# Performance work log

Measured on AMD Instinct MI355X. Metric: run time of the kernel, lower is better.

The kernel has to match this reference:

```python
import jax, jax.numpy as jnp
import numpy as np

D_MODEL = 1024
NUM_EXPERTS = 16
TOP_K = 2
TOP_C = 4  # min(M, max(4, 2*K))
RANK = 64  # max(4, d_model // 16) per choose_lowrank_r
TAU = 1.0


def setup_inputs() -> dict:
    key = jax.random.key(0)
    ks = jax.random.split(key, 7)
    B = 32768
    x = jax.random.normal(ks[0], (B, D_MODEL), dtype=jnp.float32)
    # shared encoder Linear(d, d) with bias
    We = jax.random.normal(ks[1], (D_MODEL, D_MODEL), dtype=jnp.float32) / np.sqrt(D_MODEL)
    be = jnp.zeros((D_MODEL,), dtype=jnp.float32)
    # gating Linear(d, M), no bias
    Wg = jax.random.normal(ks[2], (NUM_EXPERTS, D_MODEL), dtype=jnp.float32) / np.sqrt(D_MODEL)
    # per-expert LoRA weights: U: [M, r, d], V: [M, d, r], gamma: [M]
    U = jax.random.normal(ks[3], (NUM_EXPERTS, RANK, D_MODEL), dtype=jnp.float32) / np.sqrt(D_MODEL)
    V = jax.random.normal(ks[4], (NUM_EXPERTS, D_MODEL, RANK), dtype=jnp.float32) / np.sqrt(RANK)
    gamma = jnp.ones((NUM_EXPERTS,), dtype=jnp.float32)
    return {"x": x, "We": We, "be": be, "Wg": Wg, "U": U, "V": V, "gamma": gamma}


def reference(x, We, be, Wg, U, V, gamma):
    B = x.shape[0]
    encoded = x @ We.T + be                       # [B, d]
    logits = (encoded @ Wg.T) / TAU               # [B, M]
    # Top-C candidate selection, then Top-K among candidates
    topc_vals, topc_idx = jax.lax.top_k(logits, TOP_C)          # [B, C]
    topk_vals, pos_in_c = jax.lax.top_k(topc_vals, TOP_K)       # [B, K]
    topk_idx = jnp.take_along_axis(topc_idx, pos_in_c, axis=1)  # [B, K]
    # masked stable softmax over selected logits (matches _stable_masked_softmax)
    e = jnp.exp(topk_vals - jnp.max(topk_vals, axis=1, keepdims=True))
    w = e / (jnp.sum(e, axis=1, keepdims=True) + 1e-12)
    w = jnp.where(w > 1e-12, w, 0.0)  # keep_mask: drop negligible weights
    # scatter routing weights into dense [B, M] combine matrix
    w_full = jnp.zeros((B, NUM_EXPERTS), x.dtype).at[
        jnp.arange(B)[:, None], topk_idx].add(w)
    # expert residual delta: E(x) = x + gamma * V @ silu(U @ x)
    hidden = jax.nn.silu(jnp.einsum('bd,mrd->bmr', encoded, U))  # [B, M, r]
    delta = jnp.einsum('bmr,mdr,bm->bd', hidden, V, w_full * gamma[None, :])
    # y = encoded + sum_k w_k * (E_k(encoded) - encoded); sum_k w_k = 1
    return encoded + delta
```

## Files before the change

kernel.cpp:

```cpp
#include <hip/hip_runtime.h>
#include <stdint.h>

#define B_TOK 32768
#define DM 1024
#define NEXP 16
#define RK 64
#define NPAIR 256
#define TPT 64
#define HT 128
#define GRID_CMB 3072
#define GRID_HID 544
#define MAXTILE 1024

typedef unsigned short u16;
typedef __bf16 bf16x8 __attribute__((ext_vector_type(8)));
typedef float f32x4 __attribute__((ext_vector_type(4)));

__device__ __forceinline__ u16 f2bf(float f) {
  union { float f; uint32_t u; } v; v.f = f;
  return (u16)((v.u + 0x7fffu + ((v.u >> 16) & 1u)) >> 16);
}
__device__ __forceinline__ float bf2f(u16 u) {
  union { uint32_t i; float f; } v; v.i = ((uint32_t)u) << 16; return v.f;
}

__device__ __forceinline__ void gload_lds16(const void* g, void* l) {
  __builtin_amdgcn_global_load_lds(
      (const __attribute__((address_space(1))) void*)g,
      (__attribute__((address_space(3))) void*)l, 16, 0, 0);
}

__global__ void k_convert3(const float* __restrict__ s0, u16* __restrict__ d0,
                           const float* __restrict__ s1, u16* __restrict__ d1,
                           const float* __restrict__ s2, u16* __restrict__ d2) {
  const int seg = blockIdx.x >> 8;
  const int bid = blockIdx.x & 255;
  const float* src = (seg == 0) ? s0 : (seg == 1) ? s1 : s2;
  u16* dst = (seg == 0) ? d0 : (seg == 1) ? d1 : d2;
  int i = bid * 256 + threadIdx.x;
  #pragma unroll
  for (int v = 0; v < 4; ++v) {
    int idx = i + v * 65536;
    float4 f = reinterpret_cast<const float4*>(src)[idx];
    ushort4 o;
    o.x = f2bf(f.x); o.y = f2bf(f.y); o.z = f2bf(f.z); o.w = f2bf(f.w);
    reinterpret_cast<ushort4*>(dst)[idx] = o;
  }
}

__global__ void k_wgeff(const float* __restrict__ Wg, const float* __restrict__ We,
                        const float* __restrict__ be,
                        float* __restrict__ Wgeff, float* __restrict__ gbias) {
  int e = blockIdx.y;
  int d = blockIdx.x * 256 + threadIdx.x;
  double acc = 0.0;
  for (int k = 0; k < DM; ++k)
    acc += (double)Wg[e * DM + k] * (double)We[k * DM + d];
  Wgeff[e * DM + d] = (float)acc;
  if (blockIdx.x == 0 && threadIdx.x == 0) {
    double s = 0.0;
    for (int k = 0; k < DM; ++k) s += (double)be[k] * (double)Wg[e * DM + k];
    gbias[e] = (float)s;
  }
}

#define GT 64
#define GD 128

__global__ __launch_bounds__(256) void k_gating(
    const float* __restrict__ x, u16* __restrict__ x_bf,
    const float* __restrict__ Wgeff, const float* __restrict__ gbias,
    const float* __restrict__ gamma,
    int* __restrict__ tk_pid, float* __restrict__ tk_w0, float* __restrict__ tk_w1,
    int* __restrict__ counts_p, int* __restrict__ counts_e) {
  __shared__ float xs[GT][GD + 4];
  __shared__ float wsd[NEXP][GD + 4];
  __shared__ float lg[GT][NEXP + 2];
  __shared__ int bcnt[NPAIR];
  __shared__ int bexp[NEXP];
  const int tid = threadIdx.x;
  const int tok0 = blockIdx.x * GT;
  const int t0 = (tid >> 3) * 2;
  const int e0 = (tid & 7) * 2;
  bcnt[tid] = 0;
  if (tid < NEXP) bexp[tid] = 0;

  double acc00 = 0.0, acc01 = 0.0, acc10 = 0.0, acc11 = 0.0;

  for (int c = 0; c < DM; c += GD) {
    __syncthreads();
    #pragma unroll
    for (int v = 0; v < (GT * GD / 4) / 256; ++v) {
      int idx = tid + v * 256;
      int r = idx >> 5, cc = idx & 31;
      float4 v4 = *reinterpret_cast<const float4*>(x + (size_t)(tok0 + r) * DM + c + cc * 4);
      *reinterpret_cast<float4*>(&xs[r][cc * 4]) = v4;
      ushort4 o;
      o.x = f2bf(v4.x); o.y = f2bf(v4.y); o.z = f2bf(v4.z); o.w = f2bf(v4.w);
      *reinterpret_cast<ushort4*>(x_bf + (size_t)(tok0 + r) * DM + c + cc * 4) = o;
    }
    #pragma unroll
    for (int v = 0; v < (NEXP * GD / 4) / 256; ++v) {
      int idx = tid + v * 256;
      int r = idx >> 5, cc = idx & 31;
      *reinterpret_cast<float4*>(&wsd[r][cc * 4]) =
          *reinterpret_cast<const float4*>(Wgeff + (size_t)r * DM + c + cc * 4);
    }
    __syncthreads();
    #pragma unroll 8
    for (int d = 0; d < GD; d += 4) {
      float4 xa = *reinterpret_cast<const float4*>(&xs[t0][d]);
      float4 xb = *reinterpret_cast<const float4*>(&xs[t0 + 1][d]);
      float4 wa = *reinterpret_cast<const float4*>(&wsd[e0][d]);
      float4 wb = *reinterpret_cast<const float4*>(&wsd[e0 + 1][d]);
      acc00 += (double)xa.x * wa.x + (double)xa.y * wa.y + (double)xa.z * wa.z + (double)xa.w * wa.w;
      acc01 += (double)xa.x * wb.x + (double)xa.y * wb.y + (double)xa.z * wb.z + (double)xa.w * wb.w;
      acc10 += (double)xb.x * wa.x + (double)xb.y * wa.y + (double)xb.z * wa.z + (double)xb.w * wa.w;
      acc11 += (double)xb.x * wb.x + (double)xb.y * wb.y + (double)xb.z * wb.z + (double)xb.w * wb.w;
    }
  }

  lg[t0][e0]         = (float)(acc00 + (double)gbias[e0]);
  lg[t0][e0 + 1]     = (float)(acc01 + (double)gbias[e0 + 1]);
  lg[t0 + 1][e0]     = (float)(acc10 + (double)gbias[e0]);
  lg[t0 + 1][e0 + 1] = (float)(acc11 + (double)gbias[e0 + 1]);
  __syncthreads();

  if (tid < GT) {
    int tok = tok0 + tid;
    float v0 = lg[tid][0]; int i0 = 0;
    #pragma unroll
    for (int j = 1; j < NEXP; ++j)
      if (lg[tid][j] > v0) { v0 = lg[tid][j]; i0 = j; }
    float v1 = -3.4e38f; int i1 = 0;
    #pragma unroll
    for (int j = 0; j < NEXP; ++j) {
      if (j == i0) continue;
      if (lg[tid][j] > v1) { v1 = lg[tid][j]; i1 = j; }
    }
    float e1 = expf(v1 - v0);
    float denom = 1.0f + e1 + 1e-12f;
    float w0 = 1.0f / denom, w1 = e1 / denom;
    if (!(w0 > 1e-12f)) w0 = 0.0f;
    if (!(w1 > 1e-12f)) w1 = 0.0f;
    int pid = i0 * 16 + i1;
    tk_pid[tok] = pid;
    tk_w0[tok] = w0 * gamma[i0];
    tk_w1[tok] = w1 * gamma[i1];
    atomicAdd(&bcnt[pid], 1);
    atomicAdd(&bexp[i0], 1);
    atomicAdd(&bexp[i1], 1);
  }
  __syncthreads();
  if (bcnt[tid] > 0) atomicAdd(&counts_p[tid], bcnt[tid]);
  if (tid < NEXP && bexp[tid] > 0) atomicAdd(&counts_e[tid], bexp[tid]);
}

__global__ __launch_bounds__(NPAIR) void k_scan(
    const int* __restrict__ counts_p, const int* __restrict__ counts_e,
    int* __restrict__ offs_p, int* __restrict__ curs_p,
    int* __restrict__ offs_e, int* __restrict__ curs_e,
    int* __restrict__ tp_pair, int* __restrict__ tp_loc, int* __restrict__ n_tp,
    int* __restrict__ th_exp, int* __restrict__ th_loc, int* __restrict__ n_th) {
  __shared__ int sc[NPAIR], st[NPAIR];
  __shared__ int seb[NEXP + 1], thb[NEXP + 1];
  const int tid = threadIdx.x;
  const int c = counts_p[tid];
  const int nt = (c + TPT - 1) / TPT;
  sc[tid] = c; st[tid] = nt;
  __syncthreads();
  for (int s = 1; s < NPAIR; s <<= 1) {
    int vc = 0, vt = 0;
    if (tid >= s) { vc = sc[tid - s]; vt = st[tid - s]; }
    __syncthreads();
    sc[tid] += vc; st[tid] += vt;
    __syncthreads();
  }
  const int offc = sc[tid] - c;
  const int offt = st[tid] - nt;
  offs_p[tid] = offc;
  curs_p[tid] = offc;
  if (tid == NPAIR - 1) { offs_p[NPAIR] = sc[tid]; n_tp[0] = st[tid]; }
  for (int q = 0; q < nt; ++q) { tp_pair[offt + q] = tid; tp_loc[offt + q] = q * TPT; }

  if (tid == 0) {
    int s = 0, s2 = 0;
    for (int e = 0; e < NEXP; ++e) {
      seb[e] = s; thb[e] = s2;
      int ce = counts_e[e];
      s += ce; s2 += (ce + HT - 1) / HT;
    }
    seb[NEXP] = s; thb[NEXP] = s2;
    n_th[0] = s2;
  }
  __syncthreads();
  if (tid <= NEXP) offs_e[tid] = seb[tid];
  if (tid < NEXP) {
    curs_e[tid] = seb[tid];
    int ce = counts_e[tid];
    int ntt = (ce + HT - 1) / HT;
    for (int q = 0; q < ntt; ++q) { th_exp[thb[tid] + q] = tid; th_loc[thb[tid] + q] = q * HT; }
  }
}

__global__ __launch_bounds__(256) void k_scatter(
    const int* __restrict__ tk_pid, const float* __restrict__ tk_w0,
    const float* __restrict__ tk_w1,
    int* __restrict__ curs_p, int* __restrict__ curs_e,
    int* __restrict__ a_tok, int* __restrict__ a_h0,
    int* __restrict__ a_h1,
    int* __restrict__ e_tok, float* __restrict__ e_w) {
  __shared__ int hp[NPAIR];
  __shared__ int he[NEXP];
  __shared__ int bp[NPAIR];
  __shared__ int beB[NEXP];
  const int tid = threadIdx.x;
  const int tok = blockIdx.x * 256 + tid;
  hp[tid] = 0;
  if (tid < NEXP) he[tid] = 0;
  __syncthreads();

  const int pid = tk_pid[tok];
  const int i0 = pid >> 4, i1 = pid & 15;
  const int rp = atomicAdd(&hp[pid], 1);
  const int r0 = atomicAdd(&he[i0], 1);
  const int r1 = atomicAdd(&he[i1], 1);
  __syncthreads();

  if (hp[tid] > 0) bp[tid] = atomicAdd(&curs_p[tid], hp[tid]);
  if (tid < NEXP && he[tid] > 0) beB[tid] = atomicAdd(&curs_e[tid], he[tid]);
  __syncthreads();

  const int posp = bp[pid] + rp;
  const int pos0 = beB[i0] + r0;
  const int pos1 = beB[i1] + r1;
  a_tok[posp] = tok;
  a_h0[posp] = pos0;
  a_h1[posp] = pos1;
  e_tok[pos0] = tok; e_w[pos0] = tk_w0[tok];
  e_tok[pos1] = tok; e_w[pos1] = tk_w1[tok];
}

__global__ __launch_bounds__(256) void k_encoder(
    const u16* __restrict__ A, const u16* __restrict__ Bm,
    const float* __restrict__ bias, u16* __restrict__ Cb) {
  __shared__ __align__(16) u16 As0[128 * 64];
  __shared__ __align__(16) u16 Bs0[128 * 64];
  __shared__ __align__(16) u16 As1[128 * 64];
  __shared__ __align__(16) u16 Bs1[128 * 64];
  const int nwg = gridDim.x * gridDim.y;
  const int orig = blockIdx.y * gridDim.x + blockIdx.x;
  const int qq = nwg >> 3;
  const int swz = (orig & 7) * qq + (orig >> 3);
  const int m0 = (swz / gridDim.x) * 128, n0 = (swz % gridDim.x) * 128;
  const int tid = threadIdx.x;
  const int lane = tid & 63, wave = tid >> 6;
  const int wr = wave >> 1, wc = wave & 1;
  const int lrow = lane & 15, lhi = lane >> 4;

  f32x4 acc[4][4];
  #pragma unroll
  for (int i = 0; i < 4; ++i)
    #pragma unroll
    for (int j = 0; j < 4; ++j) acc[i][j] = (f32x4){0.f, 0.f, 0.f, 0.f};

  const u16* gA0; const u16* gA1; const u16* gA2; const u16* gA3;
  const u16* gB0; const u16* gB1; const u16* gB2; const u16* gB3;
  int dOf0, dOf1, dOf2, dOf3;
  {
    int slot, row, c, sc;
    slot = tid;         row = slot >> 3; c = slot & 7; sc = (c ^ (row & 7)) * 8;
    gA0 = A + (size_t)(m0 + row) * DM + sc; gB0 = Bm + (size_t)(n0 + row) * DM + sc; dOf0 = slot * 8;
    slot = tid + 256;   row = slot >> 3; c = slot & 7; sc = (c ^ (row & 7)) * 8;
    gA1 = A + (size_t)(m0 + row) * DM + sc; gB1 = Bm + (size_t)(n0 + row) * DM + sc; dOf1 = slot * 8;
    slot = tid + 512;   row = slot >> 3; c = slot & 7; sc = (c ^ (row & 7)) * 8;
    gA2 = A + (size_t)(m0 + row) * DM + sc; gB2 = Bm + (size_t)(n0 + row) * DM + sc; dOf2 = slot * 8;
    slot = tid + 768;   row = slot >> 3; c = slot & 7; sc = (c ^ (row & 7)) * 8;
    gA3 = A + (size_t)(m0 + row) * DM + sc; gB3 = Bm + (size_t)(n0 + row) * DM + sc; dOf3 = slot * 8;
  }

  const int rk0 = ((0 + lhi) ^ (lrow & 7)) * 8;
  const int rk1 = ((4 + lhi) ^ (lrow & 7)) * 8;

  auto STAGE = [&](u16* Ad, u16* Bd, int k0) {
    gload_lds16(gA0 + k0, Ad + dOf0);
    gload_lds16(gA1 + k0, Ad + dOf1);
    gload_lds16(gA2 + k0, Ad + dOf2);
    gload_lds16(gA3 + k0, Ad + dOf3);
    gload_lds16(gB0 + k0, Bd + dOf0);
    gload_lds16(gB1 + k0, Bd + dOf1);
    gload_lds16(gB2 + k0, Bd + dOf2);
    gload_lds16(gB3 + k0, Bd + dOf3);
  };
  auto COMPUTE = [&](const u16* Ar, const u16* Br) {
    #pragma unroll
    for (int kk = 0; kk < 2; ++kk) {
      const int rk = kk ? rk1 : rk0;
      bf16x8 a[4], b[4];
      #pragma unroll
      for (int mi = 0; mi < 4; ++mi)
        a[mi] = *reinterpret_cast<const bf16x8*>(&Ar[(wr * 64 + mi * 16 + lrow) * 64 + rk]);
      #pragma unroll
      for (int nj = 0; nj < 4; ++nj)
        b[nj] = *reinterpret_cast<const bf16x8*>(&Br[(wc * 64 + nj * 16 + lrow) * 64 + rk]);
      #pragma unroll
      for (int mi = 0; mi < 4; ++mi)
        #pragma unroll
        for (int nj = 0; nj < 4; ++nj)
          acc[mi][nj] = __builtin_amdgcn_mfma_f32_16x16x32_bf16(a[mi], b[nj], acc[mi][nj], 0, 0, 0);
    }
  };

  STAGE(As0, Bs0, 0);
  #pragma unroll
  for (int i = 0; i < 8; ++i) {
    STAGE(As1, Bs1, i * 128 + 64);
    asm volatile("s_waitcnt vmcnt(8)" ::: "memory");
    __builtin_amdgcn_s_barrier();
    COMPUTE(As0, Bs0);
    __builtin_amdgcn_s_barrier();
    if (i < 7) {
      STAGE(As0, Bs0, i * 128 + 128);
      asm volatile("s_waitcnt vmcnt(8)" ::: "memory");
    } else {
      asm volatile("s_waitcnt vmcnt(0)" ::: "memory");
    }
    __builtin_amdgcn_s_barrier();
    COMPUTE(As1, Bs1);
    __builtin_amdgcn_s_barrier();
  }

  const int orow = lhi * 4, ocol = lrow;
  #pragma unroll
  for (int mi = 0; mi < 4; ++mi) {
    #pragma unroll
    for (int nj = 0; nj < 4; ++nj) {
      int gcol = n0 + wc * 64 + nj * 16 + ocol;
      float bv = bias[gcol];
      #pragma unroll
      for (int r = 0; r < 4; ++r) {
        int grow = m0 + wr * 64 + mi * 16 + orow + r;
        Cb[(size_t)grow * DM + gcol] = f2bf(acc[mi][nj][r] + bv);
      }
    }
  }
}

__global__ __launch_bounds__(256) void k_hidden(
    const u16* __restrict__ Enc, const u16* __restrict__ Ub,
    const int* __restrict__ offs_e, const int* __restrict__ th_exp,
    const int* __restrict__ th_loc, const int* __restrict__ n_th,
    const int* __restrict__ e_tok, const float* __restrict__ e_w,
    u16* __restrict__ Hws) {
  const int bswz = (blockIdx.x & 7) * (GRID_HID >> 3) + (blockIdx.x >> 3);
  if (bswz >= n_th[0]) return;
  const int e = th_exp[bswz];
  const int loc0 = th_loc[bswz];
  const int base = offs_e[e];
  const int cnt = offs_e[e + 1] - base;
  const int tid = threadIdx.x;
  const int lane = tid & 63, wave = tid >> 6;
  const int lrow = lane & 15;
  const int lkb = (lane >> 4) * 16;

  __shared__ float s_ew[HT];
  __shared__ __align__(16) u16 Us[64 * 512];
  if (tid < HT) {
    int i = loc0 + tid;
    s_ew[tid] = (i < cnt) ? e_w[base + i] : 0.0f;
  }

  const u16* aP[2];
  #pragma unroll
  for (int mi = 0; mi < 2; ++mi) {
    int ridx = loc0 + wave * 32 + mi * 16 + lrow;
    int v = ridx < cnt;
    int tok = e_tok[base + (v ? ridx : 0)];
    aP[mi] = Enc + (size_t)tok * DM + (lane >> 4) * 8;
  }

  f32x4 acc[2][4];
  #pragma unroll
  for (int i = 0; i < 2; ++i)
    #pragma unroll
    for (int j = 0; j < 4; ++j) acc[i][j] = (f32x4){0.f, 0.f, 0.f, 0.f};

  const char* Ue = (const char*)(Ub + (size_t)e * RK * DM);

  for (int half = 0; half < 2; ++half) {
    __syncthreads();
    #pragma unroll
    for (int it = 0; it < 16; ++it) {
      int D = (tid + it * 256) * 16;
      int row = D >> 10, bo = D & 1023;
      int sbo = bo ^ ((row & 7) << 4);
      gload_lds16(Ue + (size_t)row * 2048 + half * 1024 + sbo, ((char*)Us) + D);
    }
    __syncthreads();
    #pragma unroll 4
    for (int step = 0; step < 16; ++step) {
      const int k0 = half * 512 + step * 32;
      bf16x8 b[4];
      #pragma unroll
      for (int nj = 0; nj < 4; ++nj) {
        int n = nj * 16 + lrow;
        int bofs = n * 1024 + ((step * 64 + lkb) ^ ((n & 7) << 4));
        b[nj] = *reinterpret_cast<const bf16x8*>(((const char*)Us) + bofs);
      }
      bf16x8 a0 = *reinterpret_cast<const bf16x8*>(aP[0] + k0);
      bf16x8 a1 = *reinterpret_cast<const bf16x8*>(aP[1] + k0);
      #pragma unroll
      for (int nj = 0; nj < 4; ++nj) {
        acc[0][nj] = __builtin_amdgcn_mfma_f32_16x16x32_bf16(a0, b[nj], acc[0][nj], 0, 0, 0);
        acc[1][nj] = __builtin_amdgcn_mfma_f32_16x16x32_bf16(a1, b[nj], acc[1][nj], 0, 0, 0);
      }
    }
  }

  #pragma unroll
  for (int mi = 0; mi < 2; ++mi)
    #pragma unroll
    for (int nj = 0; nj < 4; ++nj)
      #pragma unroll
      for (int rr = 0; rr < 4; ++rr) {
        int rloc = wave * 32 + mi * 16 + (lane >> 4) * 4 + rr;
        if (loc0 + rloc < cnt) {
          float z = acc[mi][nj][rr];
          float h = z / (1.0f + expf(-z)) * s_ew[rloc];
          Hws[(size_t)(base + loc0 + rloc) * RK + nj * 16 + (lane & 15)] = f2bf(h);
        }
      }
}

__global__ __launch_bounds__(256) void k_combine(
    const u16* __restrict__ Enc, const u16* __restrict__ Vb,
    const u16* __restrict__ Hws, const int* __restrict__ offs_p,
    const int* __restrict__ tp_pair, const int* __restrict__ tp_loc,
    const int* __restrict__ n_tp, const int* __restrict__ a_tok,
    const int* __restrict__ a_h0, const int* __restrict__ a_h1,
    float* __restrict__ Out) {
  const int bswz = (blockIdx.x & 7) * (GRID_CMB >> 3) + (blockIdx.x >> 3);
  const int t = bswz >> 2;
  const int p = bswz & 3;
  if (t >= n_tp[0]) return;
  const int pid = tp_pair[t];
  const int pe0 = pid >> 4, pe1 = pid & 15;
  const int base = offs_p[pid];
  const int cnt = offs_p[pid + 1] - base;
  const int loc0 = tp_loc[t];
  const int tid = threadIdx.x;
  const int lane = tid & 63, wave = tid >> 6;

  __shared__ int s_tok[TPT];
  __shared__ int s_h0[TPT];
  __shared__ int s_h1[TPT];
  __shared__ int s_val[TPT];
  if (tid < TPT) {
    int idx = loc0 + tid;
    int v = idx < cnt;
    int pp = base + (v ? idx : 0);
    s_val[tid] = v;
    s_tok[tid] = a_tok[pp];
    s_h0[tid] = a_h0[pp];
    s_h1[tid] = a_h1[pp];
  }
  __syncthreads();

  const int lrow = lane & 15, lk = (lane >> 4) * 8;
  const int col0 = p * 256 + wave * 64;

  bf16x8 hb[4][4];
  #pragma unroll
  for (int kk = 0; kk < 4; ++kk)
    #pragma unroll
    for (int tf = 0; tf < 4; ++tf) {
      int tok = tf * 16 + lrow;
      int hidx = (kk < 2) ? s_h0[tok] : s_h1[tok];
      hb[kk][tf] = *reinterpret_cast<const bf16x8*>(
          Hws + (size_t)hidx * RK + (kk & 1) * 32 + lk);
    }

  ushort4 encv[4][4];
  #pragma unroll
  for (int mi = 0; mi < 4; ++mi)
    #pragma unroll
    for (int tf = 0; tf < 4; ++tf) {
      int tok = tf * 16 + (lane & 15);
      int d = col0 + mi * 16 + (lane >> 4) * 4;
      encv[mi][tf] = *reinterpret_cast<const ushort4*>(Enc + (size_t)s_tok[tok] * DM + d);
    }

  const u16* V0 = Vb + (size_t)pe0 * DM * RK;
  const u16* V1 = Vb + (size_t)pe1 * DM * RK;

  f32x4 acc2[4][4];
  #pragma unroll
  for (int i = 0; i < 4; ++i)
    #pragma unroll
    for (int j = 0; j < 4; ++j) acc2[i][j] = (f32x4){0.f, 0.f, 0.f, 0.f};

  #pragma unroll
  for (int kk = 0; kk < 4; ++kk) {
    const u16* Vsel = (kk < 2) ? V0 : V1;
    const int kof = (kk & 1) * 32 + lk;
    #pragma unroll
    for (int mi = 0; mi < 4; ++mi) {
      int d = col0 + mi * 16 + lrow;
      bf16x8 va = *reinterpret_cast<const bf16x8*>(Vsel + (size_t)d * RK + kof);
      #pragma unroll
      for (int tf = 0; tf < 4; ++tf)
        acc2[mi][tf] = __builtin_amdgcn_mfma_f32_16x16x32_bf16(va, hb[kk][tf], acc2[mi][tf], 0, 0, 0);
    }
  }

  #pragma unroll
  for (int mi = 0; mi < 4; ++mi)
    #pragma unroll
    for (int tf = 0; tf < 4; ++tf) {
      int tok = tf * 16 + (lane & 15);
      if (!s_val[tok]) continue;
      int d = col0 + mi * 16 + (lane >> 4) * 4;
      size_t ro = (size_t)s_tok[tok] * DM + d;
      ushort4 ev = encv[mi][tf];
      float4 o;
      o.x = acc2[mi][tf][0] + bf2f(ev.x);
      o.y = acc2[mi][tf][1] + bf2f(ev.y);
      o.z = acc2[mi][tf][2] + bf2f(ev.z);
      o.w = acc2[mi][tf][3] + bf2f(ev.w);
      *reinterpret_cast<float4*>(Out + ro) = o;
    }
}

extern "C" void kernel_launch(void* const* d_in, const int* in_sizes, int n_in,
                              void* d_out, int out_size, void* d_ws, size_t ws_size,
                              hipStream_t stream) {
  const float* x = (const float*)d_in[0];
  const float* We = (const float*)d_in[1];
  const float* be = (const float*)d_in[2];
  const float* Wg = (const float*)d_in[3];
  const float* U = (const float*)d_in[4];
  const float* V = (const float*)d_in[5];
  const float* gamma = (const float*)d_in[6];
  float* Out = (float*)d_out;

  char* ws = (char*)d_ws;
  size_t off = 0;
  auto alloc = [&](size_t bytes) -> void* {
    void* p = ws + off;
    off += (bytes + 255) & ~(size_t)255;
    return p;
  };
  u16* x_bf   = (u16*)alloc((size_t)B_TOK * DM * 2);
  u16* enc_bf = (u16*)alloc((size_t)B_TOK * DM * 2);
  u16* We_bf  = (u16*)alloc((size_t)DM * DM * 2);
  u16* U_bf   = (u16*)alloc((size_t)NEXP * RK * DM * 2);
  u16* V_bf   = (u16*)alloc((size_t)NEXP * DM * RK * 2);
  u16* Hws    = (u16*)alloc(((size_t)2 * B_TOK + HT) * RK * 2);
  float* Wgeff = (float*)alloc((size_t)NEXP * DM * 4);
  float* gbias = (float*)alloc(NEXP * 4);
  int* tk_pid  = (int*)alloc((size_t)B_TOK * 4);
  float* tk_w0 = (float*)alloc((size_t)B_TOK * 4);
  float* tk_w1 = (float*)alloc((size_t)B_TOK * 4);
  int* counts_p = (int*)alloc(NPAIR * 4);
  int* counts_e = (int*)alloc(NEXP * 4);
  int* offs_p   = (int*)alloc((NPAIR + 1) * 4);
  int* curs_p   = (int*)alloc(NPAIR * 4);
  int* offs_e   = (int*)alloc((NEXP + 1) * 4);
  int* curs_e   = (int*)alloc(NEXP * 4);
  int* tp_pair  = (int*)alloc(MAXTILE * 4);
  int* tp_loc   = (int*)alloc(MAXTILE * 4);
  int* n_tp     = (int*)alloc(256);
  int* th_exp   = (int*)alloc(MAXTILE * 4);
  int* th_loc   = (int*)alloc(MAXTILE * 4);
  int* n_th     = (int*)alloc(256);
  int* a_tok   = (int*)alloc((size_t)B_TOK * 4);
  int* a_h0    = (int*)alloc((size_t)B_TOK * 4);
  int* a_h1    = (int*)alloc((size_t)B_TOK * 4);
  int* e_tok   = (int*)alloc(((size_t)2 * B_TOK + HT) * 4);
  float* e_w   = (float*)alloc(((size_t)2 * B_TOK + HT) * 4);
  (void)ws_size; (void)in_sizes; (void)n_in; (void)out_size;

  hipMemsetAsync(counts_p, 0, NPAIR * 4, stream);
  hipMemsetAsync(counts_e, 0, NEXP * 4, stream);

  k_convert3<<<768, 256, 0, stream>>>(We, We_bf, U, U_bf, V, V_bf);
  k_wgeff<<<dim3(4, 16), 256, 0, stream>>>(Wg, We, be, Wgeff, gbias);
  k_gating<<<B_TOK / GT, 256, 0, stream>>>(x, x_bf, Wgeff, gbias, gamma,
                                           tk_pid, tk_w0, tk_w1, counts_p, counts_e);
  k_scan<<<1, NPAIR, 0, stream>>>(counts_p, counts_e, offs_p, curs_p, offs_e, curs_e,
                                  tp_pair, tp_loc, n_tp, th_exp, th_loc, n_th);
  k_scatter<<<B_TOK / 256, 256, 0, stream>>>(tk_pid, tk_w0, tk_w1, curs_p, curs_e,
                                             a_tok, a_h0, a_h1, e_tok, e_w);
  k_encoder<<<dim3(DM / 128, B_TOK / 128), 256, 0, stream>>>(x_bf, We_bf, be, enc_bf);
  k_hidden<<<GRID_HID, 256, 0, stream>>>(enc_bf, U_bf, offs_e, th_exp, th_loc, n_th,
                                         e_tok, e_w, Hws);
  k_combine<<<GRID_CMB, 256, 0, stream>>>(enc_bf, V_bf, Hws, offs_p, tp_pair, tp_loc,
                                          n_tp, a_tok, a_h0, a_h1, Out);
}
```

Before: 360.9 us.

## Split Wg·We fp64 product over K chunks and fuse into weight-convert kernel

The gating-weight precompute Wg·We was a 64-block fp64 kernel with a serial 1024-long dot product per thread, leaving most of the GPU idle. It is now split into 4 K-chunks with 4 independent accumulators, run as 256 extra blocks inside the bf16 weight-conversion launch, and finished by a small reduction kernel. The intent is to shorten this serial prologue through more parallelism and overlap with the conversion, at the cost of a 512 KB fp64 partial buffer and an extra reduction pass.

Result: faster. 320.9 us, median of 2 (-11.1%).

```diff
diff --git a/kernel.cpp b/kernel.cpp
--- a/kernel.cpp
+++ b/kernel.cpp
@@ -30,37 +30,60 @@
       (__attribute__((address_space(3))) void*)l, 16, 0, 0);
 }
 
-__global__ void k_convert3(const float* __restrict__ s0, u16* __restrict__ d0,
-                           const float* __restrict__ s1, u16* __restrict__ d1,
-                           const float* __restrict__ s2, u16* __restrict__ d2) {
-  const int seg = blockIdx.x >> 8;
-  const int bid = blockIdx.x & 255;
-  const float* src = (seg == 0) ? s0 : (seg == 1) ? s1 : s2;
-  u16* dst = (seg == 0) ? d0 : (seg == 1) ? d1 : d2;
-  int i = bid * 256 + threadIdx.x;
-  #pragma unroll
-  for (int v = 0; v < 4; ++v) {
-    int idx = i + v * 65536;
-    float4 f = reinterpret_cast<const float4*>(src)[idx];
-    ushort4 o;
-    o.x = f2bf(f.x); o.y = f2bf(f.y); o.z = f2bf(f.z); o.w = f2bf(f.w);
-    reinterpret_cast<ushort4*>(dst)[idx] = o;
-  }
-}
-
-__global__ void k_wgeff(const float* __restrict__ Wg, const float* __restrict__ We,
+__global__ void k_prep(const float* __restrict__ s0, u16* __restrict__ d0,
+                       const float* __restrict__ s1, u16* __restrict__ d1,
+                       const float* __restrict__ s2, u16* __restrict__ d2,
+                       const float* __restrict__ Wg, const float* __restrict__ We,
+                       double* __restrict__ Wpart) {
+  const int b = blockIdx.x;
+  if (b < 768) {
+    const int seg = b >> 8;
+    const int bid = b & 255;
+    const float* src = (seg == 0) ? s0 : (seg == 1) ? s1 : s2;
+    u16* dst = (seg == 0) ? d0 : (seg == 1) ? d1 : d2;
+    int i = bid * 256 + threadIdx.x;
+    #pragma unroll
+    for (int v = 0; v < 4; ++v) {
+      int idx = i + v * 65536;
+      float4 f = reinterpret_cast<const float4*>(src)[idx];
+      ushort4 o;
+      o.x = f2bf(f.x); o.y = f2bf(f.y); o.z = f2bf(f.z); o.w = f2bf(f.w);
+      reinterpret_cast<ushort4*>(dst)[idx] = o;
+    }
+  } else {
+    const int pb = b - 768;
+    const int kc = pb >> 6;
+    const int rem = pb & 63;
+    const int e = rem >> 2;
+    const int bx = rem & 3;
+    const int d = bx * 256 + threadIdx.x;
+    const int kbase = kc * 256;
+    double a0 = 0.0, a1 = 0.0, a2 = 0.0, a3 = 0.0;
+    for (int k = 0; k < 256; k += 4) {
+      int kk = kbase + k;
+      a0 += (double)Wg[e * DM + kk]     * (double)We[(size_t)kk * DM + d];
+      a1 += (double)Wg[e * DM + kk + 1] * (double)We[(size_t)(kk + 1) * DM + d];
+      a2 += (double)Wg[e * DM + kk + 2] * (double)We[(size_t)(kk + 2) * DM + d];
+      a3 += (double)Wg[e * DM + kk + 3] * (double)We[(size_t)(kk + 3) * DM + d];
+    }
+    Wpart[((size_t)kc * NEXP + e) * DM + d] = (a0 + a1) + (a2 + a3);
+  }
+}
+
+__global__ void k_wgred(const double* __restrict__ Wpart, const float* __restrict__ Wg,
                         const float* __restrict__ be,
                         float* __restrict__ Wgeff, float* __restrict__ gbias) {
-  int e = blockIdx.y;
-  int d = blockIdx.x * 256 + threadIdx.x;
-  double acc = 0.0;
-  for (int k = 0; k < DM; ++k)
-    acc += (double)Wg[e * DM + k] * (double)We[k * DM + d];
-  Wgeff[e * DM + d] = (float)acc;
+  const int e = blockIdx.y;
+  const int d = blockIdx.x * 256 + threadIdx.x;
+  double s = 0.0;
+  #pragma unroll
+  for (int kc = 0; kc < 4; ++kc)
+    s += Wpart[((size_t)kc * NEXP + e) * DM + d];
+  Wgeff[e * DM + d] = (float)s;
   if (blockIdx.x == 0 && threadIdx.x == 0) {
-    double s = 0.0;
-    for (int k = 0; k < DM; ++k) s += (double)be[k] * (double)Wg[e * DM + k];
-    gbias[e] = (float)s;
+    double g = 0.0;
+    for (int k = 0; k < DM; ++k) g += (double)be[k] * (double)Wg[e * DM + k];
+    gbias[e] = (float)g;
   }
 }
 
@@ -556,6 +579,7 @@
   u16* U_bf   = (u16*)alloc((size_t)NEXP * RK * DM * 2);
   u16* V_bf   = (u16*)alloc((size_t)NEXP * DM * RK * 2);
   u16* Hws    = (u16*)alloc(((size_t)2 * B_TOK + HT) * RK * 2);
+  double* Wpart = (double*)alloc((size_t)4 * NEXP * DM * 8);
   float* Wgeff = (float*)alloc((size_t)NEXP * DM * 4);
   float* gbias = (float*)alloc(NEXP * 4);
   int* tk_pid  = (int*)alloc((size_t)B_TOK * 4);
@@ -583,8 +607,8 @@
   hipMemsetAsync(counts_p, 0, NPAIR * 4, stream);
   hipMemsetAsync(counts_e, 0, NEXP * 4, stream);
 
-  k_convert3<<<768, 256, 0, stream>>>(We, We_bf, U, U_bf, V, V_bf);
-  k_wgeff<<<dim3(4, 16), 256, 0, stream>>>(Wg, We, be, Wgeff, gbias);
+  k_prep<<<1024, 256, 0, stream>>>(We, We_bf, U, U_bf, V, V_bf, Wg, We, Wpart);
+  k_wgred<<<dim3(4, 16), 256, 0, stream>>>(Wpart, Wg, be, Wgeff, gbias);
   k_gating<<<B_TOK / GT, 256, 0, stream>>>(x, x_bf, Wgeff, gbias, gamma,
                                            tk_pid, tk_w0, tk_w1, counts_p, counts_e);
   k_scan<<<1, NPAIR, 0, stream>>>(counts_p, counts_e, offs_p, curs_p, offs_e, curs_e,
```
